# Kernel tuning notes

Hardware: AMD Instinct MI355X
Metric: run time of the kernel (lower is better)

## Reference

```python
import jax, jax.numpy as jnp
import numpy as np

MAX_LEN = 200
MAX_K = 3
ITERATION = 3
NEG_PAD = -2.0 ** 16 + 1.0


def setup_inputs() -> dict:
    key = jax.random.key(0)
    k1, k2, k3, k4 = jax.random.split(key, 4)
    B, L, D_in, D_out = 1024, MAX_LEN, 128, 128
    low_capsule = jax.random.normal(k1, (B, L, D_in), dtype=jnp.float32)
    B_matrix = jax.random.normal(k2, (1, MAX_K, L), dtype=jnp.float32)
    S_matrix = jax.random.normal(k3, (D_in, D_out), dtype=jnp.float32)
    # lengths in [1, MAX_LEN]; at least one row hits MAX_LEN so max(seq_len)==MAX_LEN
    seq_len = jax.random.randint(k4, (B, 1), 1, MAX_LEN + 1, dtype=jnp.int64)
    seq_len = seq_len.at[0, 0].set(MAX_LEN)
    return {"low_capsule": low_capsule, "B_matrix": B_matrix,
            "S_matrix": S_matrix, "seq_len": seq_len}


def squash(x):
    # torch code: norm over dim=1 (the capsule axis), keepdim
    sq = jnp.sum(jnp.square(x), axis=1, keepdims=True)
    scale = sq / (1.0 + sq) / jnp.sqrt(sq + 1e-9)
    return scale * x


def reference(low_capsule, B_matrix, S_matrix, seq_len):
    # low_capsule: [B, L, D_in], B_matrix: [1, K, L], S_matrix: [D_in, D_out], seq_len: [B, 1]
    # mask: [B, K, L] (seq_len tiled over K via broadcasting)
    mask = jnp.arange(MAX_LEN)[None, None, :] < seq_len[:, :, None]
    # bilinear projection is loop-invariant (same math as recomputing each iter)
    low_new = jnp.einsum('bld,de->ble', low_capsule, S_matrix)  # [B, L, D_out]
    high = None
    for _ in range(ITERATION):
        logits = jnp.where(mask, B_matrix, jnp.float32(NEG_PAD))  # [B, K, L]
        W = jax.nn.softmax(logits, axis=-1)
        high = squash(jnp.einsum('bkl,ble->bke', W, low_new))  # [B, K, D_out]
        # agreement, summed over batch with keepdim -> [1, K, L]
        B_delta = jnp.einsum('bke,ble->kl', high, low_new)[None]
        B_matrix = B_matrix + B_delta
    return high
```

## Files before the change

### kernel.cpp

```cpp
#include <hip/hip_runtime.h>
#include <math.h>

#define BATCH 1024
#define SEQ   200
#define DIN   128
#define DOUT  128
#define HALF  64
#define PSTR  608

typedef __attribute__((ext_vector_type(8))) short short8;
typedef __attribute__((ext_vector_type(4))) float f32x4;

__device__ __forceinline__ void async_copy16(const void* g, void* l) {
    __builtin_amdgcn_global_load_lds((const __attribute__((address_space(1))) void*)g,
                                     (__attribute__((address_space(3))) void*)l,
                                     16, 0, 0);
}

__device__ __forceinline__ unsigned pack_split(float f) {
    unsigned u = __float_as_uint(f);
    unsigned r = u + 0x8000u;
    unsigned hi = r >> 16;
    float hf = __uint_as_float(r & 0xffff0000u);
    unsigned lo = __float_as_uint(f - hf) >> 16;
    return (hi << 16) | lo;
}

__device__ __forceinline__ void split2(float f, short& h, short& l) {
    unsigned u = __float_as_uint(f);
    unsigned r = u + 0x8000u;
    h = (short)(r >> 16);
    float hf = __uint_as_float(r & 0xffff0000u);
    l = (short)(__float_as_uint(f - hf) >> 16);
}

__device__ __forceinline__ float unpk(unsigned u) {
    return __uint_as_float(u & 0xffff0000u) + __uint_as_float(u << 16);
}

__global__ __launch_bounds__(256) void k_presplit(const float* __restrict__ S,
                                                  short* __restrict__ Sp) {
    int g = blockIdx.x * 256 + threadIdx.x;
    int j = g & 7, lane = (g >> 3) & 63, kt = (g >> 9) & 3, nt = g >> 11;
    int k = kt * 32 + (lane >> 4) * 8 + j;
    int n = nt * 16 + (lane & 15);
    short h, l;
    split2(S[k * DOUT + n], h, l);
    Sp[g] = h;
    Sp[16384 + g] = l;
}

__global__ __launch_bounds__(512, 4) void k_gemm(const float* __restrict__ A,
                                                 const short* __restrict__ Sp,
                                                 unsigned* __restrict__ outp) {
    __shared__ short sSp[32768];
    const int t = threadIdx.x;
    const int w = t >> 6, lane = t & 63;
    const int q = lane >> 4, c = lane & 15;
    const long rowb = (long)blockIdx.x * 256 + w * 32;

    float4 araw[4][2][2];
#pragma unroll
    for (int kt = 0; kt < 4; ++kt)
#pragma unroll
        for (int mt = 0; mt < 2; ++mt) {
            const float* ap = A + (rowb + mt * 16 + c) * DIN + kt * 32 + q * 8;
            araw[kt][mt][0] = *(const float4*)ap;
            araw[kt][mt][1] = *(const float4*)(ap + 4);
        }

#pragma unroll
    for (int i = 0; i < 8; ++i) {
        const int g = w * 8 + i;
        async_copy16(Sp + g * 512 + lane * 8, &sSp[g * 512]);
    }

    short8 ah[4][2], al[4][2];
#pragma unroll
    for (int kt = 0; kt < 4; ++kt)
#pragma unroll
        for (int mt = 0; mt < 2; ++mt) {
            float av[8];
            *(float4*)&av[0] = araw[kt][mt][0];
            *(float4*)&av[4] = araw[kt][mt][1];
#pragma unroll
            for (int j = 0; j < 8; ++j) {
                short h, l;
                split2(av[j], h, l);
                ah[kt][mt][j] = h; al[kt][mt][j] = l;
            }
        }

    f32x4 acc[2][8];
    const f32x4 zz = {0.f, 0.f, 0.f, 0.f};
#pragma unroll
    for (int mt = 0; mt < 2; ++mt)
#pragma unroll
        for (int nt = 0; nt < 8; ++nt) acc[mt][nt] = zz;

    __syncthreads();

#pragma unroll
    for (int kt = 0; kt < 4; ++kt)
#pragma unroll
        for (int nt = 0; nt < 8; ++nt) {
            const int fo = ((nt * 4 + kt) * 64 + lane) * 8;
            short8 sh = *(const short8*)&sSp[fo];
            short8 sl = *(const short8*)&sSp[16384 + fo];
#pragma unroll
            for (int mt = 0; mt < 2; ++mt) {
                acc[mt][nt] = __builtin_amdgcn_mfma_f32_16x16x32_bf16(ah[kt][mt], sh, acc[mt][nt], 0, 0, 0);
                acc[mt][nt] = __builtin_amdgcn_mfma_f32_16x16x32_bf16(al[kt][mt], sh, acc[mt][nt], 0, 0, 0);
                acc[mt][nt] = __builtin_amdgcn_mfma_f32_16x16x32_bf16(ah[kt][mt], sl, acc[mt][nt], 0, 0, 0);
            }
        }
#pragma unroll
    for (int mt = 0; mt < 2; ++mt)
#pragma unroll
        for (int nt = 0; nt < 8; ++nt) {
            long r0 = rowb + mt * 16 + q * 4;
#pragma unroll
            for (int r = 0; r < 4; ++r)
                outp[(r0 + r) * DOUT + nt * 16 + c] = pack_split(acc[mt][nt][r]);
        }
}

__global__ __launch_bounds__(256, 6) void k_iter(
    const unsigned* __restrict__ lowp,
    const float* __restrict__ Bm,
    const int* __restrict__ seq,
    const float* __restrict__ acc0, const float* __restrict__ acc1,
    float* __restrict__ part,
    float* __restrict__ out, int iter) {
    __shared__ float sW[SEQ * 4];
    __shared__ float pB[4][3][HALF];
    __shared__ float sH[3][HALF];

    const int t = threadIdx.x;
    const int lane = t & 63, w = t >> 6;
    const int b = blockIdx.x >> 1, half = blockIdx.x & 1;
    const unsigned* lp = lowp + (size_t)b * (SEQ * DIN) + half * HALF;
    const int n = seq[b];

    if (w < 3) {
        const int k = w;
        float vv[4], m = -INFINITY;
#pragma unroll
        for (int i = 0; i < 4; ++i) {
            int l = lane + 64 * i;
            bool inb = (l < SEQ);
            float v = inb ? Bm[k * SEQ + l] : 0.f;
            if (iter >= 1 && inb) v += acc0[k * SEQ + l];
            if (iter >= 2 && inb) v += acc1[k * SEQ + l];
            vv[i] = (l < n) ? v : -INFINITY;
            if (l < n) m = fmaxf(m, v);
        }
        for (int off = 32; off; off >>= 1) m = fmaxf(m, __shfl_xor(m, off, 64));
        float s = 0.f, pv[4];
#pragma unroll
        for (int i = 0; i < 4; ++i) {
            pv[i] = (vv[i] == -INFINITY) ? 0.f : expf(vv[i] - m);
            s += pv[i];
        }
        for (int off = 32; off; off >>= 1) s += __shfl_xor(s, off, 64);
        float rs = 1.f / s;
#pragma unroll
        for (int i = 0; i < 4; ++i) {
            int l = lane + 64 * i;
            if (l < SEQ) sW[l * 4 + k] = pv[i] * rs;
        }
    }
    __syncthreads();

    {
        const int e = lane;
        const unsigned* col = lp + e;
        float h0 = 0.f, h1 = 0.f, h2 = 0.f;
#pragma unroll 10
        for (int i = 0; i < 50; ++i) {
            int l = w * 50 + i;
            float4 wv = *(const float4*)&sW[l * 4];
            float f = unpk(col[(size_t)l * DIN]);
            h0 = fmaf(wv.x, f, h0);
            h1 = fmaf(wv.y, f, h1);
            h2 = fmaf(wv.z, f, h2);
        }
        pB[w][0][e] = h0; pB[w][1][e] = h1; pB[w][2][e] = h2;
    }
    __syncthreads();

    if (t < HALF) {
        float g0 = pB[0][0][t] + pB[1][0][t] + pB[2][0][t] + pB[3][0][t];
        float g1 = pB[0][1][t] + pB[1][1][t] + pB[2][1][t] + pB[3][1][t];
        float g2 = pB[0][2][t] + pB[1][2][t] + pB[2][2][t] + pB[3][2][t];
        float sq = g0 * g0 + g1 * g1 + g2 * g2;
        float scale = sq / (1.f + sq) / sqrtf(sq + 1e-9f);
        g0 *= scale; g1 *= scale; g2 *= scale;
        if (iter == 2) {
            size_t o = (size_t)b * 3 * DOUT + half * HALF + t;
            out[o] = g0; out[o + DOUT] = g1; out[o + 2 * DOUT] = g2;
        } else {
            sH[0][t] = g0; sH[1][t] = g1; sH[2][t] = g2;
        }
    }
    if (iter == 2) return;
    __syncthreads();

    if (t < SEQ) {
        const int l = t;
        const unsigned* row = lp + (size_t)l * DIN;
        float d0 = 0.f, d1 = 0.f, d2 = 0.f;
#pragma unroll
        for (int j = 0; j < 16; ++j) {
            uint4 u = *(const uint4*)&row[4 * j];
            float4 x0 = *(const float4*)&sH[0][4 * j];
            float4 x1 = *(const float4*)&sH[1][4 * j];
            float4 x2 = *(const float4*)&sH[2][4 * j];
            float f0 = unpk(u.x), f1 = unpk(u.y), f2 = unpk(u.z), f3 = unpk(u.w);
            d0 += x0.x * f0 + x0.y * f1 + x0.z * f2 + x0.w * f3;
            d1 += x1.x * f0 + x1.y * f1 + x1.z * f2 + x1.w * f3;
            d2 += x2.x * f0 + x2.y * f1 + x2.z * f2 + x2.w * f3;
        }
        float* pp = part + (size_t)blockIdx.x * PSTR;
        pp[l] = d0;
        pp[SEQ + l] = d1;
        pp[2 * SEQ + l] = d2;
    }
}

__global__ __launch_bounds__(256) void k_reduce(const float* __restrict__ part,
                                                float* __restrict__ accN) {
    __shared__ float sP[4][4];
    const int t = threadIdx.x, lane = t & 63, w = t >> 6;
    const int c4 = blockIdx.x * 4;
    float sx = 0.f, sy = 0.f, sz = 0.f, sw = 0.f;
#pragma unroll
    for (int i = 0; i < 8; ++i) {
        float4 v = *(const float4*)&part[(size_t)(t + 256 * i) * PSTR + c4];
        sx += v.x; sy += v.y; sz += v.z; sw += v.w;
    }
#pragma unroll
    for (int off = 1; off < 64; off <<= 1) {
        sx += __shfl_xor(sx, off, 64);
        sy += __shfl_xor(sy, off, 64);
        sz += __shfl_xor(sz, off, 64);
        sw += __shfl_xor(sw, off, 64);
    }
    if (lane == 0) { sP[w][0] = sx; sP[w][1] = sy; sP[w][2] = sz; sP[w][3] = sw; }
    __syncthreads();
    if (t < 4)
        accN[c4 + t] = sP[0][t] + sP[1][t] + sP[2][t] + sP[3][t];
}

extern "C" void kernel_launch(void* const* d_in, const int* in_sizes, int n_in,
                              void* d_out, int out_size, void* d_ws, size_t ws_size,
                              hipStream_t stream) {
    const float* low_capsule = (const float*)d_in[0];
    const float* B_matrix    = (const float*)d_in[1];
    const float* S_matrix    = (const float*)d_in[2];
    const int*   seq_len     = (const int*)d_in[3];
    float* out = (float*)d_out;

    unsigned* lowp = (unsigned*)d_ws;
    short* Sp      = (short*)(lowp + (size_t)BATCH * SEQ * DOUT);
    float* acc0    = (float*)(Sp + 32768);
    float* acc1    = acc0 + 640;
    float* part    = acc1 + 640;

    k_presplit<<<64, 256, 0, stream>>>(S_matrix, Sp);
    k_gemm<<<(BATCH * SEQ) / 256, 512, 0, stream>>>(low_capsule, Sp, lowp);

    k_iter<<<2 * BATCH, 256, 0, stream>>>(lowp, B_matrix, seq_len, acc0, acc1, part, out, 0);
    k_reduce<<<150, 256, 0, stream>>>(part, acc0);
    k_iter<<<2 * BATCH, 256, 0, stream>>>(lowp, B_matrix, seq_len, acc0, acc1, part, out, 1);
    k_reduce<<<150, 256, 0, stream>>>(part, acc1);
    k_iter<<<2 * BATCH, 256, 0, stream>>>(lowp, B_matrix, seq_len, acc0, acc1, part, out, 2);
}
```

Baseline: 299.1 us.

## Persistent double-buffered GEMM and full-row per-batch routing blocks

The GEMM becomes a persistent kernel of 512 blocks. Each wave processes 3-4 row tiles with double-buffered register prefetch of A, so the S split is loaded into LDS once per block instead of once per 256 rows. The routing iteration kernel now handles a full batch row (all 128 columns) per block instead of splitting it into halves. This halves the softmax recomputation and the partial-sum count that the reduce kernel has to sum. In exchange, each k_iter block has more per-thread work and register pressure, and the GEMM has fewer blocks, which lowers parallelism.

```diff
diff --git a/kernel.cpp b/kernel.cpp
--- a/kernel.cpp
+++ b/kernel.cpp
@@ -5,7 +5,6 @@
 #define SEQ   200
 #define DIN   128
 #define DOUT  128
-#define HALF  64
 #define PSTR  608
 
 typedef __attribute__((ext_vector_type(8))) short short8;
@@ -50,82 +49,104 @@
     Sp[16384 + g] = l;
 }
 
-__global__ __launch_bounds__(512, 4) void k_gemm(const float* __restrict__ A,
+__global__ __launch_bounds__(256, 2) void k_gemm(const float* __restrict__ A,
                                                  const short* __restrict__ Sp,
                                                  unsigned* __restrict__ outp) {
     __shared__ short sSp[32768];
     const int t = threadIdx.x;
     const int w = t >> 6, lane = t & 63;
     const int q = lane >> 4, c = lane & 15;
-    const long rowb = (long)blockIdx.x * 256 + w * 32;
-
-    float4 araw[4][2][2];
-#pragma unroll
-    for (int kt = 0; kt < 4; ++kt)
-#pragma unroll
-        for (int mt = 0; mt < 2; ++mt) {
-            const float* ap = A + (rowb + mt * 16 + c) * DIN + kt * 32 + q * 8;
-            araw[kt][mt][0] = *(const float4*)ap;
-            araw[kt][mt][1] = *(const float4*)(ap + 4);
-        }
-
-#pragma unroll
-    for (int i = 0; i < 8; ++i) {
-        const int g = w * 8 + i;
+
+#pragma unroll
+    for (int i = 0; i < 16; ++i) {
+        const int g = w * 16 + i;
         async_copy16(Sp + g * 512 + lane * 8, &sSp[g * 512]);
     }
 
-    short8 ah[4][2], al[4][2];
-#pragma unroll
-    for (int kt = 0; kt < 4; ++kt)
-#pragma unroll
-        for (int mt = 0; mt < 2; ++mt) {
-            float av[8];
-            *(float4*)&av[0] = araw[kt][mt][0];
-            *(float4*)&av[4] = araw[kt][mt][1];
-#pragma unroll
-            for (int j = 0; j < 8; ++j) {
-                short h, l;
-                split2(av[j], h, l);
-                ah[kt][mt][j] = h; al[kt][mt][j] = l;
+    float4 bufA[4][2][2], bufB[4][2][2];
+
+    auto LOADA = [&](float4 (&buf)[4][2][2], long rowb) {
+#pragma unroll
+        for (int kt = 0; kt < 4; ++kt)
+#pragma unroll
+            for (int mt = 0; mt < 2; ++mt) {
+                const float* ap = A + (rowb + mt * 16 + c) * DIN + kt * 32 + q * 8;
+                buf[kt][mt][0] = *(const float4*)ap;
+                buf[kt][mt][1] = *(const float4*)(ap + 4);
             }
-        }
-
-    f32x4 acc[2][8];
-    const f32x4 zz = {0.f, 0.f, 0.f, 0.f};
-#pragma unroll
-    for (int mt = 0; mt < 2; ++mt)
-#pragma unroll
-        for (int nt = 0; nt < 8; ++nt) acc[mt][nt] = zz;
-
-    __syncthreads();
-
-#pragma unroll
-    for (int kt = 0; kt < 4; ++kt)
-#pragma unroll
-        for (int nt = 0; nt < 8; ++nt) {
-            const int fo = ((nt * 4 + kt) * 64 + lane) * 8;
-            short8 sh = *(const short8*)&sSp[fo];
-            short8 sl = *(const short8*)&sSp[16384 + fo];
+    };
+
+    auto COMPUTE = [&](float4 (&buf)[4][2][2], long rowb) {
+        short8 ah[4][2], al[4][2];
+#pragma unroll
+        for (int kt = 0; kt < 4; ++kt)
 #pragma unroll
             for (int mt = 0; mt < 2; ++mt) {
-                acc[mt][nt] = __builtin_amdgcn_mfma_f32_16x16x32_bf16(ah[kt][mt], sh, acc[mt][nt], 0, 0, 0);
-                acc[mt][nt] = __builtin_amdgcn_mfma_f32_16x16x32_bf16(al[kt][mt], sh, acc[mt][nt], 0, 0, 0);
-                acc[mt][nt] = __builtin_amdgcn_mfma_f32_16x16x32_bf16(ah[kt][mt], sl, acc[mt][nt], 0, 0, 0);
+                float av[8];
+                *(float4*)&av[0] = buf[kt][mt][0];
+                *(float4*)&av[4] = buf[kt][mt][1];
+#pragma unroll
+                for (int j = 0; j < 8; ++j) {
+                    short h, l;
+                    split2(av[j], h, l);
+                    ah[kt][mt][j] = h; al[kt][mt][j] = l;
+                }
             }
-        }
-#pragma unroll
-    for (int mt = 0; mt < 2; ++mt)
-#pragma unroll
-        for (int nt = 0; nt < 8; ++nt) {
-            long r0 = rowb + mt * 16 + q * 4;
-#pragma unroll
-            for (int r = 0; r < 4; ++r)
-                outp[(r0 + r) * DOUT + nt * 16 + c] = pack_split(acc[mt][nt][r]);
-        }
-}
-
-__global__ __launch_bounds__(256, 6) void k_iter(
+        f32x4 acc[2][8];
+        const f32x4 zz = {0.f, 0.f, 0.f, 0.f};
+#pragma unroll
+        for (int mt = 0; mt < 2; ++mt)
+#pragma unroll
+            for (int nt = 0; nt < 8; ++nt) acc[mt][nt] = zz;
+#pragma unroll
+        for (int kt = 0; kt < 4; ++kt)
+#pragma unroll
+            for (int nt = 0; nt < 8; ++nt) {
+                const int fo = ((nt * 4 + kt) * 64 + lane) * 8;
+                short8 sh = *(const short8*)&sSp[fo];
+                short8 sl = *(const short8*)&sSp[16384 + fo];
+#pragma unroll
+                for (int mt = 0; mt < 2; ++mt) {
+                    acc[mt][nt] = __builtin_amdgcn_mfma_f32_16x16x32_bf16(ah[kt][mt], sh, acc[mt][nt], 0, 0, 0);
+                    acc[mt][nt] = __builtin_amdgcn_mfma_f32_16x16x32_bf16(al[kt][mt], sh, acc[mt][nt], 0, 0, 0);
+                    acc[mt][nt] = __builtin_amdgcn_mfma_f32_16x16x32_bf16(ah[kt][mt], sl, acc[mt][nt], 0, 0, 0);
+                }
+            }
+#pragma unroll
+        for (int mt = 0; mt < 2; ++mt)
+#pragma unroll
+            for (int nt = 0; nt < 8; ++nt) {
+                long r0 = rowb + mt * 16 + q * 4;
+#pragma unroll
+                for (int r = 0; r < 4; ++r)
+                    outp[(r0 + r) * DOUT + nt * 16 + c] = pack_split(acc[mt][nt][r]);
+            }
+    };
+
+    const int base = blockIdx.x * 4 + w;
+    const long r0 = (long)base * 32;
+    const long r1 = r0 + (long)2048 * 32;
+    const long r2 = r1 + (long)2048 * 32;
+    const long r3 = r2 + (long)2048 * 32;
+    const bool h3 = (base < 256);
+
+    LOADA(bufA, r0);
+    LOADA(bufB, r1);
+    __syncthreads();
+
+    COMPUTE(bufA, r0);
+    LOADA(bufA, r2);
+    COMPUTE(bufB, r1);
+    if (h3) {
+        LOADA(bufB, r3);
+        COMPUTE(bufA, r2);
+        COMPUTE(bufB, r3);
+    } else {
+        COMPUTE(bufA, r2);
+    }
+}
+
+__global__ __launch_bounds__(256, 4) void k_iter(
     const unsigned* __restrict__ lowp,
     const float* __restrict__ Bm,
     const int* __restrict__ seq,
@@ -133,13 +154,13 @@
     float* __restrict__ part,
     float* __restrict__ out, int iter) {
     __shared__ float sW[SEQ * 4];
-    __shared__ float pB[4][3][HALF];
-    __shared__ float sH[3][HALF];
+    __shared__ float pB[4][3][DIN];
+    __shared__ float sH[3][DIN];
 
     const int t = threadIdx.x;
     const int lane = t & 63, w = t >> 6;
-    const int b = blockIdx.x >> 1, half = blockIdx.x & 1;
-    const unsigned* lp = lowp + (size_t)b * (SEQ * DIN) + half * HALF;
+    const int b = blockIdx.x;
+    const unsigned* lp = lowp + (size_t)b * (SEQ * DIN);
     const int n = seq[b];
 
     if (w < 3) {
@@ -173,23 +194,27 @@
     __syncthreads();
 
     {
-        const int e = lane;
-        const unsigned* col = lp + e;
-        float h0 = 0.f, h1 = 0.f, h2 = 0.f;
+        const unsigned* c0 = lp + lane;
+        const unsigned* c1 = lp + 64 + lane;
+        float h0a = 0.f, h1a = 0.f, h2a = 0.f;
+        float h0b = 0.f, h1b = 0.f, h2b = 0.f;
 #pragma unroll 10
         for (int i = 0; i < 50; ++i) {
             int l = w * 50 + i;
             float4 wv = *(const float4*)&sW[l * 4];
-            float f = unpk(col[(size_t)l * DIN]);
-            h0 = fmaf(wv.x, f, h0);
-            h1 = fmaf(wv.y, f, h1);
-            h2 = fmaf(wv.z, f, h2);
-        }
-        pB[w][0][e] = h0; pB[w][1][e] = h1; pB[w][2][e] = h2;
-    }
-    __syncthreads();
-
-    if (t < HALF) {
+            float fa = unpk(c0[(size_t)l * DIN]);
+            float fb = unpk(c1[(size_t)l * DIN]);
+            h0a = fmaf(wv.x, fa, h0a); h0b = fmaf(wv.x, fb, h0b);
+            h1a = fmaf(wv.y, fa, h1a); h1b = fmaf(wv.y, fb, h1b);
+            h2a = fmaf(wv.z, fa, h2a); h2b = fmaf(wv.z, fb, h2b);
+        }
+        pB[w][0][lane] = h0a; pB[w][0][64 + lane] = h0b;
+        pB[w][1][lane] = h1a; pB[w][1][64 + lane] = h1b;
+        pB[w][2][lane] = h2a; pB[w][2][64 + lane] = h2b;
+    }
+    __syncthreads();
+
+    if (t < DIN) {
         float g0 = pB[0][0][t] + pB[1][0][t] + pB[2][0][t] + pB[3][0][t];
         float g1 = pB[0][1][t] + pB[1][1][t] + pB[2][1][t] + pB[3][1][t];
         float g2 = pB[0][2][t] + pB[1][2][t] + pB[2][2][t] + pB[3][2][t];
@@ -197,7 +222,7 @@
         float scale = sq / (1.f + sq) / sqrtf(sq + 1e-9f);
         g0 *= scale; g1 *= scale; g2 *= scale;
         if (iter == 2) {
-            size_t o = (size_t)b * 3 * DOUT + half * HALF + t;
+            size_t o = (size_t)b * 3 * DOUT + t;
             out[o] = g0; out[o + DOUT] = g1; out[o + 2 * DOUT] = g2;
         } else {
             sH[0][t] = g0; sH[1][t] = g1; sH[2][t] = g2;
@@ -207,11 +232,10 @@
     __syncthreads();
 
     if (t < SEQ) {
-        const int l = t;
-        const unsigned* row = lp + (size_t)l * DIN;
+        const unsigned* row = lp + (size_t)t * DIN;
         float d0 = 0.f, d1 = 0.f, d2 = 0.f;
 #pragma unroll
-        for (int j = 0; j < 16; ++j) {
+        for (int j = 0; j < 32; ++j) {
             uint4 u = *(const uint4*)&row[4 * j];
             float4 x0 = *(const float4*)&sH[0][4 * j];
             float4 x1 = *(const float4*)&sH[1][4 * j];
@@ -221,10 +245,10 @@
             d1 += x1.x * f0 + x1.y * f1 + x1.z * f2 + x1.w * f3;
             d2 += x2.x * f0 + x2.y * f1 + x2.z * f2 + x2.w * f3;
         }
-        float* pp = part + (size_t)blockIdx.x * PSTR;
-        pp[l] = d0;
-        pp[SEQ + l] = d1;
-        pp[2 * SEQ + l] = d2;
+        float* pp = part + (size_t)b * PSTR;
+        pp[t] = d0;
+        pp[SEQ + t] = d1;
+        pp[2 * SEQ + t] = d2;
     }
 }
 
@@ -235,7 +259,7 @@
     const int c4 = blockIdx.x * 4;
     float sx = 0.f, sy = 0.f, sz = 0.f, sw = 0.f;
 #pragma unroll
-    for (int i = 0; i < 8; ++i) {
+    for (int i = 0; i < 4; ++i) {
         float4 v = *(const float4*)&part[(size_t)(t + 256 * i) * PSTR + c4];
         sx += v.x; sy += v.y; sz += v.z; sw += v.w;
     }
@@ -268,11 +292,11 @@
     float* part    = acc1 + 640;
 
     k_presplit<<<64, 256, 0, stream>>>(S_matrix, Sp);
-    k_gemm<<<(BATCH * SEQ) / 256, 512, 0, stream>>>(low_capsule, Sp, lowp);
-
-    k_iter<<<2 * BATCH, 256, 0, stream>>>(lowp, B_matrix, seq_len, acc0, acc1, part, out, 0);
+    k_gemm<<<512, 256, 0, stream>>>(low_capsule, Sp, lowp);
+
+    k_iter<<<BATCH, 256, 0, stream>>>(lowp, B_matrix, seq_len, acc0, acc1, part, out, 0);
     k_reduce<<<150, 256, 0, stream>>>(part, acc0);
-    k_iter<<<2 * BATCH, 256, 0, stream>>>(lowp, B_matrix, seq_len, acc0, acc1, part, out, 1);
+    k_iter<<<BATCH, 256, 0, stream>>>(lowp, B_matrix, seq_len, acc0, acc1, part, out, 1);
     k_reduce<<<150, 256, 0, stream>>>(part, acc1);
-    k_iter<<<2 * BATCH, 256, 0, stream>>>(lowp, B_matrix, seq_len, acc0, acc1, part, out, 2);
-}
+    k_iter<<<BATCH, 256, 0, stream>>>(lowp, B_matrix, seq_len, acc0, acc1, part, out, 2);
+}
```

Measured after the change: 280.4 us. 6.3% less time.
